# Performance work log

Measured on AMD Instinct MI355X. Metric: run time of the kernel, lower is better.

The kernel has to match this reference:

```python
import jax, jax.numpy as jnp
import numpy as np

GROUPS = 32
EPS = 1e-6

def groupnorm(x, gamma, beta):
    b, c, h, w = x.shape
    xg = x.reshape(b, GROUPS, c // GROUPS, h, w)
    mu = xg.mean(axis=(2, 3, 4), keepdims=True)
    var = xg.var(axis=(2, 3, 4), keepdims=True)
    xn = ((xg - mu) / jnp.sqrt(var + EPS)).reshape(b, c, h, w)
    return xn * gamma[None, :, None, None] + beta[None, :, None, None]

def conv1x1(x, w, b):
    return jnp.einsum('oc,bchw->bohw', w, x) + b[None, :, None, None]

def attn_branch(xn, wq, bq, wk, bk, v_flat, scale):
    q = conv1x1(xn, wq, bq)
    k = conv1x1(xn, wk, bk)
    b_, c, h, w = q.shape
    qf = q.reshape(b_, c, h * w)   # b c n
    kf = k.reshape(b_, c, h * w)   # b c n
    scores = jnp.einsum('bci,bcj->bij', qf, kf) * scale  # b n n
    attn = jax.nn.softmax(scores, axis=2)
    out = jnp.einsum('bcj,bij->bci', v_flat, attn)       # b c n
    return out.reshape(b_, c, h, w)

def setup_inputs() -> dict:
    key = jax.random.key(0)
    ks = jax.random.split(key, 14)
    B, C, H, W = 4, 64, 64, 64
    R = C // 16  # SE reduction
    s = 0.05
    return {
        'x1': jax.random.normal(ks[0], (B, C, H, W), jnp.float32),
        'x2': jax.random.normal(ks[1], (B, C, H, W), jnp.float32),
        'se_w1': jax.random.normal(ks[2], (R, C), jnp.float32) * s,
        'se_w2': jax.random.normal(ks[3], (C, R), jnp.float32) * s,
        'gn_gamma': jnp.ones((C,), jnp.float32),
        'gn_beta': jnp.zeros((C,), jnp.float32),
        'wq': jax.random.normal(ks[4], (C, C), jnp.float32) * s,
        'bq': jnp.zeros((C,), jnp.float32),
        'wk': jax.random.normal(ks[5], (C, C), jnp.float32) * s,
        'bk': jnp.zeros((C,), jnp.float32),
        'wv': jax.random.normal(ks[6], (C, C), jnp.float32) * s,
        'bv': jnp.zeros((C,), jnp.float32),
    }

def reference(x1, x2, se_w1, se_w2, gn_gamma, gn_beta, wq, bq, wk, bk, wv, bv):
    x = x1 + x2
    # SE channel attention (ends in sigmoid), then an EXTRA sigmoid as in source
    y = x.mean(axis=(2, 3))                         # b c
    y = jax.nn.relu(y @ se_w1.T)                    # b r
    y = jax.nn.sigmoid(y @ se_w2.T)                 # b c
    se = x * y[:, :, None, None]
    ch_w = jax.nn.sigmoid(se)
    xn = groupnorm(x, gn_gamma, gn_beta)
    v = conv1x1(xn, wv, bv)
    b_, c, h, w = v.shape
    v_flat = v.reshape(b_, c, h * w)
    scale = 1.0 / jnp.sqrt(jnp.float32(c))
    # source reuses q1/k1 convs for BOTH branches
    h1 = attn_branch(groupnorm(x1, gn_gamma, gn_beta), wq, bq, wk, bk, v_flat, scale)
    h2 = attn_branch(groupnorm(x2, gn_gamma, gn_beta), wq, bq, wk, bk, v_flat, scale)
    return 2.0 * h1 * ch_w + 2.0 * h2 * (1.0 - ch_w)
```

## Files before the change

kernel.cpp:

```cpp
#include <hip/hip_runtime.h>

#define STATS_OFF 0
#define AD_OFF    5120
#define SEY_OFF   11264
#define WQB_OFF   16384
#define WKB_OFF   24576
#define WVB_OFF   32768
#define Q_OFF     40960
#define K_OFF     (Q_OFF + 4194304)
#define V_OFF     (K_OFF + 4194304)
#define PO_OFF    (V_OFF + 2097152)
#define PL_OFF    (PO_OFF + 8388608)

#define QSCALE 0.18033688f

typedef __attribute__((ext_vector_type(8))) short  short8;
typedef __attribute__((ext_vector_type(4))) float  f32x4;

__device__ inline ushort f2b(float f) {
  unsigned u = __float_as_uint(f);
  return (ushort)((u + 0x7fffu + ((u >> 16) & 1u)) >> 16);
}
__device__ inline float b2f(ushort u) { return __uint_as_float(((unsigned)u) << 16); }

__device__ inline f32x4 mfma16(short8 a, short8 b, f32x4 c) {
  return __builtin_amdgcn_mfma_f32_16x16x32_bf16(a, b, c, 0, 0, 0);
}

__device__ inline float wsum64(float v) {
  #pragma unroll
  for (int o = 32; o > 0; o >>= 1) v += __shfl_down(v, o, 64);
  return v;
}
__device__ inline float rsum16(float v) {
  v += __shfl_xor(v, 1, 16);
  v += __shfl_xor(v, 2, 16);
  v += __shfl_xor(v, 4, 16);
  v += __shfl_xor(v, 8, 16);
  return v;
}

__global__ __launch_bounds__(256) void sc_stats(const float* __restrict__ x1,
                                                const float* __restrict__ x2,
                                                float* __restrict__ stats) {
  int bc = blockIdx.x;
  const float* p1 = x1 + (size_t)bc * 4096;
  const float* p2 = x2 + (size_t)bc * 4096;
  float s1 = 0, q1 = 0, s2 = 0, q2 = 0, p12 = 0;
  for (int i = threadIdx.x; i < 4096; i += 256) {
    float a = p1[i], b = p2[i];
    s1 += a; q1 += a * a; s2 += b; q2 += b * b; p12 += a * b;
  }
  s1 = wsum64(s1); q1 = wsum64(q1); s2 = wsum64(s2); q2 = wsum64(q2); p12 = wsum64(p12);
  __shared__ float red[4][5];
  int w = threadIdx.x >> 6, ln = threadIdx.x & 63;
  if (ln == 0) { red[w][0] = s1; red[w][1] = q1; red[w][2] = s2; red[w][3] = q2; red[w][4] = p12; }
  __syncthreads();
  if (threadIdx.x < 5) {
    float acc = 0;
    #pragma unroll
    for (int ww = 0; ww < 4; ww++) acc += red[ww][threadIdx.x];
    stats[(size_t)bc * 5 + threadIdx.x] = acc;
  }
}

__global__ __launch_bounds__(256) void sc_prep(const float* __restrict__ stats,
                                               const float* __restrict__ w1,
                                               const float* __restrict__ w2,
                                               const float* __restrict__ gamma,
                                               const float* __restrict__ beta,
                                               const float* __restrict__ wq,
                                               const float* __restrict__ wk,
                                               const float* __restrict__ wv,
                                               float* __restrict__ ad, float* __restrict__ sey,
                                               ushort* __restrict__ wqb, ushort* __restrict__ wkb,
                                               ushort* __restrict__ wvb) {
  int t = threadIdx.x; int b = t >> 6, c = t & 63;
  float s1 = stats[t*5], q1 = stats[t*5+1], s2 = stats[t*5+2], q2 = stats[t*5+3], p12 = stats[t*5+4];
  float sx = s1 + s2, qx = q1 + q2 + 2.f * p12;
  __shared__ float smu[256], sS[3][256], sQ[3][256], sy[16];
  smu[t] = sx * (1.f / 4096.f);
  sS[0][t] = sx; sQ[0][t] = qx; sS[1][t] = s1; sQ[1][t] = q1; sS[2][t] = s2; sQ[2][t] = q2;
  __syncthreads();
  if (t < 16) {
    int bb = t >> 2, r = t & 3; float acc = 0.f;
    for (int cc = 0; cc < 64; cc++) acc += w1[r*64+cc] * smu[bb*64+cc];
    sy[t] = fmaxf(acc, 0.f);
  }
  __syncthreads();
  float acc = 0.f;
  #pragma unroll
  for (int r = 0; r < 4; r++) acc += w2[c*4+r] * sy[b*4+r];
  sey[t] = 1.f / (1.f + exp2f(-acc * 1.44269504f));
  int prt = t ^ 1;
  float g = gamma[c], bt = beta[c];
  #pragma unroll
  for (int s = 0; s < 3; s++) {
    float S = sS[s][t] + sS[s][prt], Q = sQ[s][t] + sQ[s][prt];
    float mean = S * (1.f / 8192.f);
    float var  = Q * (1.f / 8192.f) - mean * mean;
    float rstd = rsqrtf(var + 1e-6f);
    float a = g * rstd;
    ad[((s*256) + t)*2 + 0] = a;
    ad[((s*256) + t)*2 + 1] = bt - mean * a;
  }
  for (int i = t; i < 4096; i += 256) {
    wqb[i] = f2b(wq[i] * QSCALE);
    wkb[i] = f2b(wk[i]);
    wvb[i] = f2b(wv[i]);
  }
}

__global__ __launch_bounds__(256) void sc_proj(const float* __restrict__ x1, const float* __restrict__ x2,
    const float* __restrict__ wq, const float* __restrict__ bq,
    const float* __restrict__ wk, const float* __restrict__ bk,
    const float* __restrict__ wv, const float* __restrict__ bv,
    const float* __restrict__ ad,
    const ushort* __restrict__ wqb, const ushort* __restrict__ wkb, const ushort* __restrict__ wvb,
    ushort* __restrict__ qout, ushort* __restrict__ kout, ushort* __restrict__ vout) {
  int pt = blockIdx.x, src = blockIdx.y, b = blockIdx.z, t = threadIdx.x;
  __shared__ ushort xlds[64 * 66];
  __shared__ float sa[64], sd[64], sbias[2][64];
  if (t < 64) {
    sa[t] = ad[((src*256) + b*64 + t)*2 + 0];
    sd[t] = ad[((src*256) + b*64 + t)*2 + 1];
  }
  __syncthreads();
  int nbias = (src == 0) ? 64 : 128;
  if (t < nbias) {
    int proj = t >> 6, o = t & 63;
    const float* W  = (src == 0) ? wv : (proj == 0 ? wq : wk);
    const float* bs = (src == 0) ? bv : (proj == 0 ? bq : bk);
    float acc = bs[o];
    for (int cc = 0; cc < 64; cc++) acc += W[o*64+cc] * sd[cc];
    if (src != 0 && proj == 0) acc *= QSCALE;
    sbias[proj][o] = acc;
  }
  {
    int c = t >> 2, pq = (t & 3) * 16;
    const float* px1 = x1 + ((size_t)(b*64 + c))*4096 + pt*64 + pq;
    const float* px2 = x2 + ((size_t)(b*64 + c))*4096 + pt*64 + pq;
    float av = ad[((src*256) + b*64 + c)*2 + 0];
    #pragma unroll
    for (int k4 = 0; k4 < 4; k4++) {
      float4 v1 = *(const float4*)(px1 + 4*k4);
      float xv[4];
      if (src == 1) { xv[0]=v1.x; xv[1]=v1.y; xv[2]=v1.z; xv[3]=v1.w; }
      else {
        float4 v2 = *(const float4*)(px2 + 4*k4);
        if (src == 2) { xv[0]=v2.x; xv[1]=v2.y; xv[2]=v2.z; xv[3]=v2.w; }
        else { xv[0]=v1.x+v2.x; xv[1]=v1.y+v2.y; xv[2]=v1.z+v2.z; xv[3]=v1.w+v2.w; }
      }
      #pragma unroll
      for (int k = 0; k < 4; k++)
        xlds[(pq + 4*k4 + k)*66 + c] = f2b(av * xv[k]);
    }
  }
  __syncthreads();
  int wave = t >> 6, lane = t & 63, quad = lane >> 4, l15 = lane & 15;
  if (src == 0) {
    const ushort* ap = wvb + (wave*16 + l15)*64 + quad*8;
    short8 a0 = *(const short8*)ap;
    short8 a1 = *(const short8*)(ap + 32);
    f32x4 cinit;
    #pragma unroll
    for (int r = 0; r < 4; r++) cinit[r] = sbias[0][wave*16 + quad*4 + r];
    #pragma unroll
    for (int s = 0; s < 4; s++) {
      const ushort* bp = xlds + (s*16 + l15)*66 + quad*8;
      short8 b0 = *(const short8*)bp;
      short8 b1 = *(const short8*)(bp + 32);
      f32x4 acc = mfma16(a0, b0, cinit);
      acc = mfma16(a1, b1, acc);
      #pragma unroll
      for (int r = 0; r < 4; r++)
        vout[((size_t)(b*64 + wave*16 + quad*4 + r))*4096 + pt*64 + s*16 + l15] = f2b(acc[r]);
    }
  } else {
    int bh = b*2 + (src - 1);
    const ushort* ap = xlds + (wave*16 + l15)*66 + quad*8;
    short8 a0 = *(const short8*)ap;
    short8 a1 = *(const short8*)(ap + 32);
    #pragma unroll
    for (int proj = 0; proj < 2; proj++) {
      const ushort* Wb = proj == 0 ? wqb : wkb;
      ushort* dst = proj == 0 ? qout : kout;
      #pragma unroll
      for (int s = 0; s < 4; s++) {
        const ushort* bp = Wb + (s*16 + l15)*64 + quad*8;
        short8 b0 = *(const short8*)bp;
        short8 b1 = *(const short8*)(bp + 32);
        float bb = sbias[proj][s*16 + l15];
        f32x4 acc = {bb, bb, bb, bb};
        acc = mfma16(a0, b0, acc);
        acc = mfma16(a1, b1, acc);
        #pragma unroll
        for (int r = 0; r < 4; r++)
          dst[((size_t)bh*4096 + pt*64 + wave*16 + quad*4 + r)*64 + s*16 + l15] = f2b(acc[r]);
      }
    }
  }
}

__global__ __launch_bounds__(256) void sc_flash(const ushort* __restrict__ qg,
                                                const ushort* __restrict__ kg,
                                                const ushort* __restrict__ vg,
                                                ushort* __restrict__ po,
                                                float* __restrict__ pl) {
  int blk = blockIdx.x;
  int bh = blk & 7, rest = blk >> 3;
  int itile = rest >> 1, js = rest & 1;
  int b = bh >> 1;
  int t = threadIdx.x, wave = t >> 6, lane = t & 63, quad = lane >> 4, l15 = lane & 15;
  int i0 = itile * 64 + wave * 16;

  __shared__ ushort Klds[64 * 72];
  __shared__ ushort Vlds[64 * 72];
  __shared__ ushort Plds[4][16 * 72];

  const ushort* qp = qg + ((size_t)bh * 4096 + i0 + l15) * 64 + quad * 8;
  short8 aq0 = *(const short8*)qp;
  short8 aq1 = *(const short8*)(qp + 32);

  f32x4 O[4]; const f32x4 zero4 = {0.f, 0.f, 0.f, 0.f};
  #pragma unroll
  for (int s = 0; s < 4; s++) O[s] = zero4;
  float l[4] = {0.f, 0.f, 0.f, 0.f};

  int jr = t >> 2, c0 = (t & 3) * 16;
  const ushort* ksrc = kg + ((size_t)bh * 4096 + jr) * 64 + c0;
  ushort* kdst = Klds + jr * 72 + c0;
  const ushort* vsrc = vg + ((size_t)(b * 64 + jr)) * 4096 + c0;
  ushort* vdst = Vlds + jr * 72 + c0;

  for (int jt = 0; jt < 32; jt++) {
    int j0 = js * 2048 + jt * 64;
    __syncthreads();
    {
      const uint4* sk = (const uint4*)(ksrc + (size_t)j0 * 64);
      uint4 ka = sk[0], kb4 = sk[1];
      const uint4* sv = (const uint4*)(vsrc + j0);
      uint4 va = sv[0], vb4 = sv[1];
      *(uint4*)kdst = ka; *(uint4*)(kdst + 8) = kb4;
      *(uint4*)vdst = va; *(uint4*)(vdst + 8) = vb4;
    }
    __syncthreads();

    f32x4 S[4];
    #pragma unroll
    for (int s = 0; s < 4; s++) {
      const ushort* kbp = Klds + (s * 16 + l15) * 72 + quad * 8;
      short8 k0 = *(const short8*)kbp;
      short8 k1 = *(const short8*)(kbp + 32);
      f32x4 acc = mfma16(aq0, k0, zero4);
      S[s] = mfma16(aq1, k1, acc);
    }

    #pragma unroll
    for (int r = 0; r < 4; r++) {
      #pragma unroll
      for (int s = 0; s < 4; s++) {
        float pv = exp2f(S[s][r]);
        S[s][r] = pv;
        l[r] += pv;
      }
    }
    #pragma unroll
    for (int r = 0; r < 4; r++) {
      #pragma unroll
      for (int s = 0; s < 4; s++)
        Plds[wave][(quad * 4 + r) * 72 + s * 16 + l15] = f2b(S[s][r]);
    }
    __threadfence_block();
    short8 a0 = *(const short8*)&Plds[wave][l15 * 72 + quad * 8];
    short8 a1 = *(const short8*)&Plds[wave][l15 * 72 + quad * 8 + 32];

    #pragma unroll
    for (int s = 0; s < 4; s++) {
      const ushort* vbp = Vlds + (s * 16 + l15) * 72 + quad * 8;
      short8 v0 = *(const short8*)vbp;
      short8 v1 = *(const short8*)(vbp + 32);
      O[s] = mfma16(a0, v0, O[s]);
      O[s] = mfma16(a1, v1, O[s]);
    }
  }

  size_t slice = (size_t)(bh * 2 + js) * 4096;
  #pragma unroll
  for (int r = 0; r < 4; r++) {
    float lr = rsum16(l[r]);
    ushort* op = po + (slice + i0 + quad * 4 + r) * 64 + l15;
    #pragma unroll
    for (int s = 0; s < 4; s++) op[s * 16] = f2b(O[s][r]);
    if (l15 == 0) pl[slice + i0 + quad * 4 + r] = lr;
  }
}

__global__ __launch_bounds__(256) void sc_combine(const float* __restrict__ x1, const float* __restrict__ x2,
                                                  const ushort* __restrict__ po, const float* __restrict__ pl,
                                                  const float* __restrict__ sey,
                                                  float* __restrict__ out) {
  int itile = blockIdx.x, b = blockIdx.y, t = threadIdx.x;
  __shared__ float hl[2][64 * 65];
  #pragma unroll
  for (int head = 0; head < 2; head++) {
    int bh = b * 2 + head;
    size_t s0 = (size_t)(bh * 2 + 0) * 4096, s1 = (size_t)(bh * 2 + 1) * 4096;
    #pragma unroll
    for (int rep = 0; rep < 4; rep++) {
      int idx = rep * 256 + t;
      int i = idx >> 4, c04 = (idx & 15) * 4;
      size_t off = (size_t)(itile * 64 + i) * 64 + c04;
      uint2 u0 = *(const uint2*)(po + s0 * 64 + off);
      uint2 u1 = *(const uint2*)(po + s1 * 64 + off);
      float inv = 1.f / (pl[s0 + itile * 64 + i] + pl[s1 + itile * 64 + i]);
      ushort* p0 = (ushort*)&u0; ushort* p1 = (ushort*)&u1;
      #pragma unroll
      for (int k = 0; k < 4; k++)
        hl[head][i * 65 + c04 + k] = (b2f(p0[k]) + b2f(p1[k])) * inv;
    }
  }
  __syncthreads();
  #pragma unroll
  for (int it = 0; it < 16; it++) {
    int idx = it * 256 + t;
    int c = idx >> 6, p = idx & 63;
    size_t gi = ((size_t)(b * 64 + c)) * 4096 + itile * 64 + p;
    float xv = x1[gi] + x2[gi];
    float sig = 1.f / (1.f + exp2f(-xv * sey[b * 64 + c] * 1.44269504f));
    float h1 = hl[0][p * 65 + c], h2 = hl[1][p * 65 + c];
    out[gi] = 2.f * (h1 * sig + h2 * (1.f - sig));
  }
}

extern "C" void kernel_launch(void* const* d_in, const int* in_sizes, int n_in,
                              void* d_out, int out_size, void* d_ws, size_t ws_size,
                              hipStream_t stream) {
  (void)in_sizes; (void)n_in; (void)out_size; (void)ws_size;
  const float* x1    = (const float*)d_in[0];
  const float* x2    = (const float*)d_in[1];
  const float* se_w1 = (const float*)d_in[2];
  const float* se_w2 = (const float*)d_in[3];
  const float* gamma = (const float*)d_in[4];
  const float* beta  = (const float*)d_in[5];
  const float* wq    = (const float*)d_in[6];
  const float* bq    = (const float*)d_in[7];
  const float* wk    = (const float*)d_in[8];
  const float* bk    = (const float*)d_in[9];
  const float* wv    = (const float*)d_in[10];
  const float* bv    = (const float*)d_in[11];
  float* out = (float*)d_out;
  char* ws = (char*)d_ws;
  float*  stats = (float*)(ws + STATS_OFF);
  float*  ad    = (float*)(ws + AD_OFF);
  float*  sey   = (float*)(ws + SEY_OFF);
  ushort* wqb   = (ushort*)(ws + WQB_OFF);
  ushort* wkb   = (ushort*)(ws + WKB_OFF);
  ushort* wvb   = (ushort*)(ws + WVB_OFF);
  ushort* qb    = (ushort*)(ws + Q_OFF);
  ushort* kb    = (ushort*)(ws + K_OFF);
  ushort* vb    = (ushort*)(ws + V_OFF);
  ushort* pob   = (ushort*)(ws + PO_OFF);
  float*  plb   = (float*)(ws + PL_OFF);

  sc_stats  <<<256, 256, 0, stream>>>(x1, x2, stats);
  sc_prep   <<<1, 256, 0, stream>>>(stats, se_w1, se_w2, gamma, beta, wq, wk, wv,
                                    ad, sey, wqb, wkb, wvb);
  sc_proj   <<<dim3(64, 3, 4), 256, 0, stream>>>(x1, x2, wq, bq, wk, bk, wv, bv, ad,
                                                 wqb, wkb, wvb, qb, kb, vb);
  sc_flash  <<<1024, 256, 0, stream>>>(qb, kb, vb, pob, plb);
  sc_combine<<<dim3(64, 4), 256, 0, stream>>>(x1, x2, pob, plb, sey, out);
}
```

Baseline: 184.4 us.

## Restructure flash kernel for 32-row tiles and register P/V, split stats/combine

The flash kernel now processes 32 query rows per wave, halving the grid. It loads V directly from global memory into registers and keeps P in registers via the 16x16x16 bf16 MFMA, removing the V and P LDS staging and reusing each K tile over twice as many rows. Stats and combine are split across more blocks, and the projection bias is precomputed once in the prep kernel. The bf16 rounding changes from round-to-nearest-even to round-half-up, which slightly alters numerics, and the register-held V tiles raise register pressure.

Measured after the change: 235.5 us. 27.8% more time.

```diff
diff --git a/kernel.cpp b/kernel.cpp
--- a/kernel.cpp
+++ b/kernel.cpp
@@ -1,12 +1,13 @@
 #include <hip/hip_runtime.h>
 
 #define STATS_OFF 0
-#define AD_OFF    5120
-#define SEY_OFF   11264
-#define WQB_OFF   16384
-#define WKB_OFF   24576
-#define WVB_OFF   32768
-#define Q_OFF     40960
+#define AD_OFF    20480
+#define SEY_OFF   26624
+#define BIAS_OFF  27648
+#define WQB_OFF   32768
+#define WKB_OFF   40960
+#define WVB_OFF   49152
+#define Q_OFF     57344
 #define K_OFF     (Q_OFF + 4194304)
 #define V_OFF     (K_OFF + 4194304)
 #define PO_OFF    (V_OFF + 2097152)
@@ -15,11 +16,23 @@
 #define QSCALE 0.18033688f
 
 typedef __attribute__((ext_vector_type(8))) short  short8;
+typedef __attribute__((ext_vector_type(4))) short  s16x4;
+typedef __attribute__((ext_vector_type(2))) unsigned int u32x2;
 typedef __attribute__((ext_vector_type(4))) float  f32x4;
 
+#if __has_builtin(__builtin_amdgcn_mfma_f32_16x16x16bf16_1k)
+#define HAS_1K 1
+#else
+#define HAS_1K 0
+#endif
+
 __device__ inline ushort f2b(float f) {
-  unsigned u = __float_as_uint(f);
-  return (ushort)((u + 0x7fffu + ((u >> 16) & 1u)) >> 16);
+  return (ushort)((__float_as_uint(f) + 0x8000u) >> 16);
+}
+__device__ inline unsigned pack2(float x, float y) {
+  unsigned ux = __float_as_uint(x) + 0x8000u;
+  unsigned uy = __float_as_uint(y) + 0x8000u;
+  return __builtin_amdgcn_perm(uy, ux, 0x07060302);
 }
 __device__ inline float b2f(ushort u) { return __uint_as_float(((unsigned)u) << 16); }
 
@@ -30,27 +43,22 @@
 __device__ inline float wsum64(float v) {
   #pragma unroll
   for (int o = 32; o > 0; o >>= 1) v += __shfl_down(v, o, 64);
-  return v;
-}
-__device__ inline float rsum16(float v) {
-  v += __shfl_xor(v, 1, 16);
-  v += __shfl_xor(v, 2, 16);
-  v += __shfl_xor(v, 4, 16);
-  v += __shfl_xor(v, 8, 16);
   return v;
 }
 
 __global__ __launch_bounds__(256) void sc_stats(const float* __restrict__ x1,
                                                 const float* __restrict__ x2,
                                                 float* __restrict__ stats) {
-  int bc = blockIdx.x;
-  const float* p1 = x1 + (size_t)bc * 4096;
-  const float* p2 = x2 + (size_t)bc * 4096;
-  float s1 = 0, q1 = 0, s2 = 0, q2 = 0, p12 = 0;
-  for (int i = threadIdx.x; i < 4096; i += 256) {
-    float a = p1[i], b = p2[i];
-    s1 += a; q1 += a * a; s2 += b; q2 += b * b; p12 += a * b;
-  }
+  int blk = blockIdx.x;
+  int bc = blk >> 2, chunk = blk & 3;
+  const float4* p1 = (const float4*)(x1 + (size_t)bc * 4096 + chunk * 1024);
+  const float4* p2 = (const float4*)(x2 + (size_t)bc * 4096 + chunk * 1024);
+  float4 a = p1[threadIdx.x], b = p2[threadIdx.x];
+  float s1 = a.x + a.y + a.z + a.w;
+  float q1 = a.x*a.x + a.y*a.y + a.z*a.z + a.w*a.w;
+  float s2 = b.x + b.y + b.z + b.w;
+  float q2 = b.x*b.x + b.y*b.y + b.z*b.z + b.w*b.w;
+  float p12 = a.x*b.x + a.y*b.y + a.z*b.z + a.w*b.w;
   s1 = wsum64(s1); q1 = wsum64(q1); s2 = wsum64(s2); q2 = wsum64(q2); p12 = wsum64(p12);
   __shared__ float red[4][5];
   int w = threadIdx.x >> 6, ln = threadIdx.x & 63;
@@ -60,7 +68,7 @@
     float acc = 0;
     #pragma unroll
     for (int ww = 0; ww < 4; ww++) acc += red[ww][threadIdx.x];
-    stats[(size_t)bc * 5 + threadIdx.x] = acc;
+    stats[(size_t)blk * 5 + threadIdx.x] = acc;
   }
 }
 
@@ -69,16 +77,22 @@
                                                const float* __restrict__ w2,
                                                const float* __restrict__ gamma,
                                                const float* __restrict__ beta,
-                                               const float* __restrict__ wq,
-                                               const float* __restrict__ wk,
-                                               const float* __restrict__ wv,
+                                               const float* __restrict__ wq, const float* __restrict__ bq,
+                                               const float* __restrict__ wk, const float* __restrict__ bk,
+                                               const float* __restrict__ wv, const float* __restrict__ bv,
                                                float* __restrict__ ad, float* __restrict__ sey,
+                                               float* __restrict__ biasbuf,
                                                ushort* __restrict__ wqb, ushort* __restrict__ wkb,
                                                ushort* __restrict__ wvb) {
   int t = threadIdx.x; int b = t >> 6, c = t & 63;
-  float s1 = stats[t*5], q1 = stats[t*5+1], s2 = stats[t*5+2], q2 = stats[t*5+3], p12 = stats[t*5+4];
+  float s1 = 0, q1 = 0, s2 = 0, q2 = 0, p12 = 0;
+  #pragma unroll
+  for (int ch = 0; ch < 4; ch++) {
+    const float* sp = stats + (size_t)(t * 4 + ch) * 5;
+    s1 += sp[0]; q1 += sp[1]; s2 += sp[2]; q2 += sp[3]; p12 += sp[4];
+  }
   float sx = s1 + s2, qx = q1 + q2 + 2.f * p12;
-  __shared__ float smu[256], sS[3][256], sQ[3][256], sy[16];
+  __shared__ float smu[256], sS[3][256], sQ[3][256], sy[16], sdd[3][256];
   smu[t] = sx * (1.f / 4096.f);
   sS[0][t] = sx; sQ[0][t] = qx; sS[1][t] = s1; sQ[1][t] = q1; sS[2][t] = s2; sQ[2][t] = q2;
   __syncthreads();
@@ -101,8 +115,24 @@
     float var  = Q * (1.f / 8192.f) - mean * mean;
     float rstd = rsqrtf(var + 1e-6f);
     float a = g * rstd;
+    float d = bt - mean * a;
     ad[((s*256) + t)*2 + 0] = a;
-    ad[((s*256) + t)*2 + 1] = bt - mean * a;
+    ad[((s*256) + t)*2 + 1] = d;
+    sdd[s][t] = d;
+  }
+  __syncthreads();
+  #pragma unroll
+  for (int k = 0; k < 5; k++) {
+    int idx = k * 256 + t;
+    const float* W; const float* bs; const float* dd; int o; float scale = 1.f;
+    if (idx < 256)      { int bb = idx >> 6; o = idx & 63; W = wv; bs = bv; dd = &sdd[0][bb*64]; }
+    else if (idx < 768) { int r = idx - 256; int bh = r >> 6; o = r & 63; W = wq; bs = bq;
+                          dd = &sdd[1 + (bh & 1)][(bh >> 1)*64]; scale = QSCALE; }
+    else                { int r = idx - 768; int bh = r >> 6; o = r & 63; W = wk; bs = bk;
+                          dd = &sdd[1 + (bh & 1)][(bh >> 1)*64]; }
+    float a2 = bs[o];
+    for (int cc = 0; cc < 64; cc++) a2 += W[o*64+cc] * dd[cc];
+    biasbuf[idx] = a2 * scale;
   }
   for (int i = t; i < 4096; i += 256) {
     wqb[i] = f2b(wq[i] * QSCALE);
@@ -112,29 +142,18 @@
 }
 
 __global__ __launch_bounds__(256) void sc_proj(const float* __restrict__ x1, const float* __restrict__ x2,
-    const float* __restrict__ wq, const float* __restrict__ bq,
-    const float* __restrict__ wk, const float* __restrict__ bk,
-    const float* __restrict__ wv, const float* __restrict__ bv,
-    const float* __restrict__ ad,
+    const float* __restrict__ ad, const float* __restrict__ biasbuf,
     const ushort* __restrict__ wqb, const ushort* __restrict__ wkb, const ushort* __restrict__ wvb,
     ushort* __restrict__ qout, ushort* __restrict__ kout, ushort* __restrict__ vout) {
   int pt = blockIdx.x, src = blockIdx.y, b = blockIdx.z, t = threadIdx.x;
   __shared__ ushort xlds[64 * 66];
-  __shared__ float sa[64], sd[64], sbias[2][64];
-  if (t < 64) {
-    sa[t] = ad[((src*256) + b*64 + t)*2 + 0];
-    sd[t] = ad[((src*256) + b*64 + t)*2 + 1];
-  }
-  __syncthreads();
-  int nbias = (src == 0) ? 64 : 128;
-  if (t < nbias) {
+  __shared__ float sbias[2][64];
+  if (t < 128) {
     int proj = t >> 6, o = t & 63;
-    const float* W  = (src == 0) ? wv : (proj == 0 ? wq : wk);
-    const float* bs = (src == 0) ? bv : (proj == 0 ? bq : bk);
-    float acc = bs[o];
-    for (int cc = 0; cc < 64; cc++) acc += W[o*64+cc] * sd[cc];
-    if (src != 0 && proj == 0) acc *= QSCALE;
-    sbias[proj][o] = acc;
+    float bb;
+    if (src == 0) bb = (proj == 0) ? biasbuf[b*64 + o] : 0.f;
+    else          bb = biasbuf[256 + (proj ? 512 : 0) + (b*2 + src - 1)*64 + o];
+    sbias[proj][o] = bb;
   }
   {
     int c = t >> 2, pq = (t & 3) * 16;
@@ -212,87 +231,136 @@
   int itile = rest >> 1, js = rest & 1;
   int b = bh >> 1;
   int t = threadIdx.x, wave = t >> 6, lane = t & 63, quad = lane >> 4, l15 = lane & 15;
-  int i0 = itile * 64 + wave * 16;
+  int i0 = itile * 128 + wave * 32;
 
   __shared__ ushort Klds[64 * 72];
-  __shared__ ushort Vlds[64 * 72];
-  __shared__ ushort Plds[4][16 * 72];
-
-  const ushort* qp = qg + ((size_t)bh * 4096 + i0 + l15) * 64 + quad * 8;
-  short8 aq0 = *(const short8*)qp;
-  short8 aq1 = *(const short8*)(qp + 32);
-
-  f32x4 O[4]; const f32x4 zero4 = {0.f, 0.f, 0.f, 0.f};
-  #pragma unroll
-  for (int s = 0; s < 4; s++) O[s] = zero4;
-  float l[4] = {0.f, 0.f, 0.f, 0.f};
-
-  int jr = t >> 2, c0 = (t & 3) * 16;
-  const ushort* ksrc = kg + ((size_t)bh * 4096 + jr) * 64 + c0;
-  ushort* kdst = Klds + jr * 72 + c0;
-  const ushort* vsrc = vg + ((size_t)(b * 64 + jr)) * 4096 + c0;
-  ushort* vdst = Vlds + jr * 72 + c0;
-
+#if !HAS_1K
+  __shared__ ushort Plds[4][32 * 72];
+#endif
+
+  const ushort* qbase = qg + ((size_t)bh * 4096 + i0 + l15) * 64 + quad * 8;
+  short8 Qb[2][2];
+  Qb[0][0] = *(const short8*)qbase;
+  Qb[0][1] = *(const short8*)(qbase + 32);
+  Qb[1][0] = *(const short8*)(qbase + 16 * 64);
+  Qb[1][1] = *(const short8*)(qbase + 16 * 64 + 32);
+
+  f32x4 O[2][4]; const f32x4 zero4 = {0.f, 0.f, 0.f, 0.f};
+  #pragma unroll
+  for (int ib = 0; ib < 2; ib++)
+    #pragma unroll
+    for (int cb = 0; cb < 4; cb++) O[ib][cb] = zero4;
+  float lsum[2] = {0.f, 0.f};
+
+  int jr = t >> 2, jc = (t & 3) * 16;
+  const ushort* ksrc = kg + ((size_t)bh * 4096 + js * 2048 + jr) * 64 + jc;
+  ushort* kdst = Klds + jr * 72 + jc;
+  const ushort* kread = Klds + l15 * 72 + quad * 8;
+#if HAS_1K
+  const ushort* vp[4];
+  #pragma unroll
+  for (int cb = 0; cb < 4; cb++)
+    vp[cb] = vg + ((size_t)(b * 64 + cb * 16 + l15)) * 4096 + js * 2048 + quad * 4;
+#else
+  const ushort* vp8[4];
+  #pragma unroll
+  for (int cb = 0; cb < 4; cb++)
+    vp8[cb] = vg + ((size_t)(b * 64 + cb * 16 + l15)) * 4096 + js * 2048 + quad * 8;
+#endif
+
+  #pragma unroll 1
   for (int jt = 0; jt < 32; jt++) {
-    int j0 = js * 2048 + jt * 64;
+    int joff = jt * 64;
     __syncthreads();
-    {
-      const uint4* sk = (const uint4*)(ksrc + (size_t)j0 * 64);
-      uint4 ka = sk[0], kb4 = sk[1];
-      const uint4* sv = (const uint4*)(vsrc + j0);
-      uint4 va = sv[0], vb4 = sv[1];
-      *(uint4*)kdst = ka; *(uint4*)(kdst + 8) = kb4;
-      *(uint4*)vdst = va; *(uint4*)(vdst + 8) = vb4;
-    }
+    uint4 k0 = *(const uint4*)ksrc;
+    uint4 k1 = *(const uint4*)(ksrc + 8);
+    ksrc += 4096;
+#if HAS_1K
+    s16x4 Vb[4][4];
+    #pragma unroll
+    for (int s = 0; s < 4; s++)
+      #pragma unroll
+      for (int cb = 0; cb < 4; cb++)
+        Vb[s][cb] = *(const s16x4*)(vp[cb] + joff + s * 16);
+#else
+    short8 Vb8[2][4];
+    #pragma unroll
+    for (int h = 0; h < 2; h++)
+      #pragma unroll
+      for (int cb = 0; cb < 4; cb++)
+        Vb8[h][cb] = *(const short8*)(vp8[cb] + joff + h * 32);
+#endif
+    *(uint4*)kdst = k0;
+    *(uint4*)(kdst + 8) = k1;
     __syncthreads();
 
-    f32x4 S[4];
+    f32x4 S[2][4];
     #pragma unroll
     for (int s = 0; s < 4; s++) {
-      const ushort* kbp = Klds + (s * 16 + l15) * 72 + quad * 8;
-      short8 k0 = *(const short8*)kbp;
-      short8 k1 = *(const short8*)(kbp + 32);
-      f32x4 acc = mfma16(aq0, k0, zero4);
-      S[s] = mfma16(aq1, k1, acc);
-    }
-
-    #pragma unroll
-    for (int r = 0; r < 4; r++) {
+      short8 ka0 = *(const short8*)(kread + s * 1152);
+      short8 ka1 = *(const short8*)(kread + s * 1152 + 32);
+      #pragma unroll
+      for (int ib = 0; ib < 2; ib++) {
+        f32x4 acc = mfma16(ka0, Qb[ib][0], zero4);
+        S[ib][s] = mfma16(ka1, Qb[ib][1], acc);
+      }
+    }
+#if HAS_1K
+    s16x4 Pb[2][4];
+#endif
+    #pragma unroll
+    for (int ib = 0; ib < 2; ib++) {
       #pragma unroll
       for (int s = 0; s < 4; s++) {
-        float pv = exp2f(S[s][r]);
-        S[s][r] = pv;
-        l[r] += pv;
+        float p0 = exp2f(S[ib][s][0]);
+        float p1 = exp2f(S[ib][s][1]);
+        float p2 = exp2f(S[ib][s][2]);
+        float p3 = exp2f(S[ib][s][3]);
+        lsum[ib] += (p0 + p1) + (p2 + p3);
+#if HAS_1K
+        u32x2 wpk = {pack2(p0, p1), pack2(p2, p3)};
+        Pb[ib][s] = __builtin_bit_cast(s16x4, wpk);
+#else
+        ushort* pw = &Plds[wave][(ib * 16 + l15) * 72 + s * 16 + quad * 4];
+        pw[0] = f2b(p0); pw[1] = f2b(p1); pw[2] = f2b(p2); pw[3] = f2b(p3);
+#endif
       }
     }
-    #pragma unroll
-    for (int r = 0; r < 4; r++) {
-      #pragma unroll
-      for (int s = 0; s < 4; s++)
-        Plds[wave][(quad * 4 + r) * 72 + s * 16 + l15] = f2b(S[s][r]);
-    }
+#if HAS_1K
+    #pragma unroll
+    for (int s = 0; s < 4; s++)
+      #pragma unroll
+      for (int ib = 0; ib < 2; ib++)
+        #pragma unroll
+        for (int cb = 0; cb < 4; cb++)
+          O[ib][cb] = __builtin_amdgcn_mfma_f32_16x16x16bf16_1k(Pb[ib][s], Vb[s][cb], O[ib][cb], 0, 0, 0);
+#else
     __threadfence_block();
-    short8 a0 = *(const short8*)&Plds[wave][l15 * 72 + quad * 8];
-    short8 a1 = *(const short8*)&Plds[wave][l15 * 72 + quad * 8 + 32];
-
-    #pragma unroll
-    for (int s = 0; s < 4; s++) {
-      const ushort* vbp = Vlds + (s * 16 + l15) * 72 + quad * 8;
-      short8 v0 = *(const short8*)vbp;
-      short8 v1 = *(const short8*)(vbp + 32);
-      O[s] = mfma16(a0, v0, O[s]);
-      O[s] = mfma16(a1, v1, O[s]);
-    }
+    #pragma unroll
+    for (int ib = 0; ib < 2; ib++) {
+      short8 pa0 = *(const short8*)&Plds[wave][(ib * 16 + l15) * 72 + quad * 8];
+      short8 pa1 = *(const short8*)&Plds[wave][(ib * 16 + l15) * 72 + quad * 8 + 32];
+      #pragma unroll
+      for (int cb = 0; cb < 4; cb++) {
+        O[ib][cb] = mfma16(pa0, Vb8[0][cb], O[ib][cb]);
+        O[ib][cb] = mfma16(pa1, Vb8[1][cb], O[ib][cb]);
+      }
+    }
+#endif
   }
 
   size_t slice = (size_t)(bh * 2 + js) * 4096;
   #pragma unroll
-  for (int r = 0; r < 4; r++) {
-    float lr = rsum16(l[r]);
-    ushort* op = po + (slice + i0 + quad * 4 + r) * 64 + l15;
-    #pragma unroll
-    for (int s = 0; s < 4; s++) op[s * 16] = f2b(O[s][r]);
-    if (l15 == 0) pl[slice + i0 + quad * 4 + r] = lr;
+  for (int ib = 0; ib < 2; ib++) {
+    float lv = lsum[ib];
+    lv += __shfl_xor(lv, 16, 64);
+    lv += __shfl_xor(lv, 32, 64);
+    if (quad == 0) pl[slice + i0 + ib * 16 + l15] = lv;
+    #pragma unroll
+    for (int cb = 0; cb < 4; cb++)
+      #pragma unroll
+      for (int r = 0; r < 4; r++)
+        po[(slice + i0 + ib * 16 + quad * 4 + r) * 64 + cb * 16 + l15] = f2b(O[ib][cb][r]);
   }
 }
 
@@ -300,35 +368,40 @@
                                                   const ushort* __restrict__ po, const float* __restrict__ pl,
                                                   const float* __restrict__ sey,
                                                   float* __restrict__ out) {
-  int itile = blockIdx.x, b = blockIdx.y, t = threadIdx.x;
-  __shared__ float hl[2][64 * 65];
+  int itile = blockIdx.x, b = blockIdx.y, ch = blockIdx.z, t = threadIdx.x;
+  __shared__ float hl[2][32 * 65];
+  __shared__ float linv[2][64];
+  if (t < 128) {
+    int head = t >> 6, i = t & 63;
+    size_t s0 = (size_t)((b * 2 + head) * 2) * 4096;
+    linv[head][i] = 1.f / (pl[s0 + itile * 64 + i] + pl[s0 + 4096 + itile * 64 + i]);
+  }
+  __syncthreads();
   #pragma unroll
   for (int head = 0; head < 2; head++) {
-    int bh = b * 2 + head;
-    size_t s0 = (size_t)(bh * 2 + 0) * 4096, s1 = (size_t)(bh * 2 + 1) * 4096;
-    #pragma unroll
-    for (int rep = 0; rep < 4; rep++) {
-      int idx = rep * 256 + t;
-      int i = idx >> 4, c04 = (idx & 15) * 4;
-      size_t off = (size_t)(itile * 64 + i) * 64 + c04;
-      uint2 u0 = *(const uint2*)(po + s0 * 64 + off);
-      uint2 u1 = *(const uint2*)(po + s1 * 64 + off);
-      float inv = 1.f / (pl[s0 + itile * 64 + i] + pl[s1 + itile * 64 + i]);
-      ushort* p0 = (ushort*)&u0; ushort* p1 = (ushort*)&u1;
-      #pragma unroll
-      for (int k = 0; k < 4; k++)
-        hl[head][i * 65 + c04 + k] = (b2f(p0[k]) + b2f(p1[k])) * inv;
-    }
-  }
-  __syncthreads();
-  #pragma unroll
-  for (int it = 0; it < 16; it++) {
+    size_t base = (size_t)((b * 2 + head) * 2) * 4096 * 64;
+    int i = t >> 2, c8 = (t & 3) * 8;
+    const ushort* p0 = po + base + (size_t)(itile * 64 + i) * 64 + ch * 32 + c8;
+    const ushort* p1 = p0 + (size_t)4096 * 64;
+    uint4 u0 = *(const uint4*)p0;
+    uint4 u1 = *(const uint4*)p1;
+    float inv = linv[head][i];
+    const ushort* us0 = (const ushort*)&u0;
+    const ushort* us1 = (const ushort*)&u1;
+    #pragma unroll
+    for (int k = 0; k < 8; k++)
+      hl[head][(c8 + k) * 65 + i] = (b2f(us0[k]) + b2f(us1[k])) * inv;
+  }
+  __syncthreads();
+  #pragma unroll
+  for (int it = 0; it < 8; it++) {
     int idx = it * 256 + t;
-    int c = idx >> 6, p = idx & 63;
+    int cl = idx >> 6, p = idx & 63;
+    int c = ch * 32 + cl;
     size_t gi = ((size_t)(b * 64 + c)) * 4096 + itile * 64 + p;
     float xv = x1[gi] + x2[gi];
     float sig = 1.f / (1.f + exp2f(-xv * sey[b * 64 + c] * 1.44269504f));
-    float h1 = hl[0][p * 65 + c], h2 = hl[1][p * 65 + c];
+    float h1 = hl[0][cl * 65 + p], h2 = hl[1][cl * 65 + p];
     out[gi] = 2.f * (h1 * sig + h2 * (1.f - sig));
   }
 }
@@ -354,6 +427,7 @@
   float*  stats = (float*)(ws + STATS_OFF);
   float*  ad    = (float*)(ws + AD_OFF);
   float*  sey   = (float*)(ws + SEY_OFF);
+  float*  biasb = (float*)(ws + BIAS_OFF);
   ushort* wqb   = (ushort*)(ws + WQB_OFF);
   ushort* wkb   = (ushort*)(ws + WKB_OFF);
   ushort* wvb   = (ushort*)(ws + WVB_OFF);
@@ -363,11 +437,12 @@
   ushort* pob   = (ushort*)(ws + PO_OFF);
   float*  plb   = (float*)(ws + PL_OFF);
 
-  sc_stats  <<<256, 256, 0, stream>>>(x1, x2, stats);
-  sc_prep   <<<1, 256, 0, stream>>>(stats, se_w1, se_w2, gamma, beta, wq, wk, wv,
-                                    ad, sey, wqb, wkb, wvb);
-  sc_proj   <<<dim3(64, 3, 4), 256, 0, stream>>>(x1, x2, wq, bq, wk, bk, wv, bv, ad,
+  sc_stats  <<<1024, 256, 0, stream>>>(x1, x2, stats);
+  sc_prep   <<<1, 256, 0, stream>>>(stats, se_w1, se_w2, gamma, beta,
+                                    wq, bq, wk, bk, wv, bv,
+                                    ad, sey, biasb, wqb, wkb, wvb);
+  sc_proj   <<<dim3(64, 3, 4), 256, 0, stream>>>(x1, x2, ad, biasb,
                                                  wqb, wkb, wvb, qb, kb, vb);
-  sc_flash  <<<1024, 256, 0, stream>>>(qb, kb, vb, pob, plb);
-  sc_combine<<<dim3(64, 4), 256, 0, stream>>>(x1, x2, pob, plb, sey, out);
-}
+  sc_flash  <<<512, 256, 0, stream>>>(qb, kb, vb, pob, plb);
+  sc_combine<<<dim3(64, 4, 2), 256, 0, stream>>>(x1, x2, pob, plb, sey, out);
+}
```
